# Kernel tuning notes

Hardware: AMD Instinct MI355X
Metric: run time of the kernel (lower is better)

Reference implementation:

```python
import jax, jax.numpy as jnp
import numpy as np

T, B = 384, 128
IN_DIM, HID, OUT_DIM = 512, 1024, 512


def _lstm_step(h, c, x_t, Wx, Wh, b):
    # x_t: [B, D], h/c: [B, H]; gates order: i, f, g, o
    gates = x_t @ Wx + h @ Wh + b  # [B, 4H]
    i, f, g, o = jnp.split(gates, 4, axis=-1)
    c_new = jax.nn.sigmoid(f) * c + jax.nn.sigmoid(i) * jnp.tanh(g)
    h_new = jax.nn.sigmoid(o) * jnp.tanh(c_new)
    return h_new, c_new


def setup_inputs() -> dict:
    key = jax.random.key(0)
    ks = jax.random.split(key, 9)
    s_in = 1.0 / np.sqrt(IN_DIM)
    s_h = 1.0 / np.sqrt(HID)
    s_o = 1.0 / np.sqrt(OUT_DIM)
    return {
        "x": jax.random.normal(ks[0], (T, B, IN_DIM), dtype=jnp.float32),
        "hidden_state": jnp.zeros((1, B, HID), dtype=jnp.float32),
        "cell_state": jnp.zeros((1, B, HID), dtype=jnp.float32),
        "enc_Wx": jax.random.normal(ks[1], (IN_DIM, 4 * HID), dtype=jnp.float32) * s_in,
        "enc_Wh": jax.random.normal(ks[2], (HID, 4 * HID), dtype=jnp.float32) * s_h,
        "enc_b": jnp.zeros((4 * HID,), dtype=jnp.float32),
        "dec_Wx": jax.random.normal(ks[3], (OUT_DIM, 4 * HID), dtype=jnp.float32) * s_o,
        "dec_Wh": jax.random.normal(ks[4], (HID, 4 * HID), dtype=jnp.float32) * s_h,
        "dec_b": jnp.zeros((4 * HID,), dtype=jnp.float32),
        "fc_W": jax.random.normal(ks[5], (HID, OUT_DIM), dtype=jnp.float32) * s_h,
        "fc_b": jnp.zeros((OUT_DIM,), dtype=jnp.float32),
    }


def reference(x, hidden_state, cell_state, enc_Wx, enc_Wh, enc_b,
              dec_Wx, dec_Wh, dec_b, fc_W, fc_b):
    # ---- encoder: run LSTM over T steps, keep only final hidden state ----
    h0, c0 = hidden_state[0], cell_state[0]  # [B, H]

    def enc_step(carry, x_t):
        h, c = carry
        h, c = _lstm_step(h, c, x_t, enc_Wx, enc_Wh, enc_b)
        return (h, c), None

    (h_enc, _), _ = jax.lax.scan(enc_step, (h0, c0), x)

    y0 = jnp.zeros((B, OUT_DIM), dtype=x.dtype)
    c_dec0 = jnp.zeros((B, HID), dtype=x.dtype)

    def dec_step(carry, _):
        y, h, c = carry
        h, c = _lstm_step(h, c, y, dec_Wx, dec_Wh, dec_b)
        y = jax.nn.softmax(h @ fc_W + fc_b, axis=-1)  # softmax over dim=2
        return (y, h, c), y

    _, output = jax.lax.scan(dec_step, (y0, h_enc, c_dec0), None, length=T)
    return output  # [T, B, OUT_DIM]
```

## Files before the change

### kernel.cpp

```cpp
#include <hip/hip_runtime.h>


#define TS 384

typedef __attribute__((ext_vector_type(8))) short bf16x8;
typedef __attribute__((ext_vector_type(4))) float f32x4;

#define WS_XR 4096u
#define XR_SLOT 262144u
#define WS_HP (WS_XR + 4u*XR_SLOT)
#define HP_BUF 524288u
#define WS_FPN (WS_HP + 2u*HP_BUF)
#define WS_TOTAL (WS_FPN + 2097152u)

__device__ __forceinline__ unsigned short bf16r(float v) {
  unsigned u = __float_as_uint(v);
  u += 0x7FFFu + ((u >> 16) & 1u);
  return (unsigned short)(u >> 16);
}
__device__ __forceinline__ float bf2f(unsigned short h) {
  return __uint_as_float(((unsigned)h) << 16);
}
__device__ __forceinline__ void split2(float v, short& hi, short& lo) {
  unsigned short h = bf16r(v);
  float r = v - bf2f(h);
  hi = (short)h; lo = (short)bf16r(r);
}
__device__ __forceinline__ float sigm(float v)  { return 1.0f / (1.0f + __expf(-v)); }
__device__ __forceinline__ float tanhfa(float v){ return 1.0f - 2.0f / (__expf(2.0f*v) + 1.0f); }

__device__ __forceinline__ void st_u64(short* p, unsigned long long v) {
  __hip_atomic_store((unsigned long long*)p, v, __ATOMIC_RELAXED, __HIP_MEMORY_SCOPE_AGENT);
}
__device__ __forceinline__ void st_f32(float* p, float v) {
  __hip_atomic_store(p, v, __ATOMIC_RELAXED, __HIP_MEMORY_SCOPE_AGENT);
}
__device__ __forceinline__ float ld_f32(const float* p) {
  return __hip_atomic_load(p, __ATOMIC_RELAXED, __HIP_MEMORY_SCOPE_AGENT);
}
__device__ __forceinline__ unsigned ldc(const unsigned* p) {
  return __hip_atomic_load(p, __ATOMIC_RELAXED, __HIP_MEMORY_SCOPE_AGENT);
}

__device__ __forceinline__ void arrive(unsigned* line) {
  asm volatile("s_waitcnt vmcnt(0)" ::: "memory");
  __syncthreads();
  if (threadIdx.x == 0)
    __hip_atomic_fetch_add(line, 1u, __ATOMIC_RELAXED, __HIP_MEMORY_SCOPE_AGENT);
}
__device__ __forceinline__ void wait4(const unsigned* base, unsigned target,
                                      bool fence, int* sDead) {
  if (threadIdx.x == 0) {
    unsigned spins = 0;
    for (;;) {
      unsigned c0 = ldc(base), c1 = ldc(base + 64);
      unsigned c2 = ldc(base + 128), c3 = ldc(base + 192);
      if (c0 >= target && c1 >= target && c2 >= target && c3 >= target) break;
      __builtin_amdgcn_s_sleep(1);
      if (++spins > (1u << 19)) { *sDead = 1; break; }
    }
    if (fence) __builtin_amdgcn_fence(__ATOMIC_ACQUIRE, "agent");
  }
  __syncthreads();
}
__device__ __forceinline__ void wait1(const unsigned* line, unsigned target,
                                      int* sDead) {
  if (threadIdx.x == 0) {
    unsigned spins = 0;
    while (ldc(line) < target) {
      __builtin_amdgcn_s_sleep(1);
      if (++spins > (1u << 19)) { *sDead = 1; break; }
    }
  }
  __syncthreads();
}

__device__ void load_gate_weights(const float* __restrict__ Wx, const float* __restrict__ Wh,
                                  int p, short* sBh, short* sBl) {
  for (int idx = threadIdx.x; idx < 24576; idx += 1024) {
    int j = idx & 7, l = (idx >> 3) & 63, kb = idx >> 9;
    int k = kb * 32 + ((l >> 4) << 3) + j;
    int c = l & 15;
    int gcol = (c >> 2) * 1024 + p * 4 + (c & 3);
    float wv = (k < 512) ? Wx[(size_t)k * 4096 + gcol]
                         : Wh[(size_t)(k - 512) * 4096 + gcol];
    short hi, lo; split2(wv, hi, lo);
    sBh[idx] = hi; sBl[idx] = lo;
  }
}
__device__ void load_fc_weights(const float* __restrict__ fcW, int kg, int cg,
                                short* sFh, short* sFl) {
  for (int idx = threadIdx.x; idx < 4096; idx += 1024) {
    int j = idx & 7, l = (idx >> 3) & 63, kb = idx >> 9;
    int unit = kg * 256 + kb * 32 + ((l >> 4) << 3) + j;
    int col = cg * 16 + (l & 15);
    short hi, lo; split2(fcW[(size_t)unit * 512 + col], hi, lo);
    sFh[idx] = hi; sFl[idx] = lo;
  }
}

__device__ __forceinline__ void gg(const short* AHs, const short* ALs,
    const short* BHs, const short* BLs, int mt, int l,
    int kbA0, int kbB0, int nkb, f32x4* acc)
{
  const bf16x8* AH = (const bf16x8*)AHs;
  const bf16x8* AL = (const bf16x8*)ALs;
  const bf16x8* BH = (const bf16x8*)BHs;
  const bf16x8* BL = (const bf16x8*)BLs;
  #pragma unroll 2
  for (int i = 0; i < nkb; i += 2) {
    int ka = kbA0 + i, kb = kbB0 + i;
    bf16x8 ah0 = AH[(ka * 8 + mt) * 64 + l];
    bf16x8 al0 = AL[(ka * 8 + mt) * 64 + l];
    bf16x8 bh0 = BH[kb * 64 + l];
    bf16x8 bl0 = BL[kb * 64 + l];
    bf16x8 ah1 = AH[((ka + 1) * 8 + mt) * 64 + l];
    bf16x8 al1 = AL[((ka + 1) * 8 + mt) * 64 + l];
    bf16x8 bh1 = BH[(kb + 1) * 64 + l];
    bf16x8 bl1 = BL[(kb + 1) * 64 + l];
    acc[0] = __builtin_amdgcn_mfma_f32_16x16x32_bf16(ah0, bh0, acc[0], 0, 0, 0);
    acc[1] = __builtin_amdgcn_mfma_f32_16x16x32_bf16(ah0, bl0, acc[1], 0, 0, 0);
    acc[2] = __builtin_amdgcn_mfma_f32_16x16x32_bf16(al0, bh0, acc[2], 0, 0, 0);
    acc[3] = __builtin_amdgcn_mfma_f32_16x16x32_bf16(ah1, bh1, acc[3], 0, 0, 0);
    acc[4] = __builtin_amdgcn_mfma_f32_16x16x32_bf16(ah1, bl1, acc[4], 0, 0, 0);
    acc[5] = __builtin_amdgcn_mfma_f32_16x16x32_bf16(al1, bh1, acc[5], 0, 0, 0);
  }
}
__device__ __forceinline__ void gg_finish(f32x4* acc, int kh, int mt, int l,
                                          float* LDSgate) {
  f32x4 s = (acc[0] + acc[3]) + ((acc[1] + acc[4]) + (acc[2] + acc[5]));
  const int col = l & 15, r0 = mt * 16 + ((l >> 4) << 2);
  float* plane = LDSgate + kh * 2176;
  #pragma unroll
  for (int j = 0; j < 4; ++j) plane[(r0 + j) * 17 + col] = s[j];
}

__device__ __forceinline__ void conv_x(const float* __restrict__ xsrc,
                                       short* dstH, short* dstL, int p, int t) {
  if (t < 32) {
    int g = p * 32 + t;
    int l = g & 63, mt = (g >> 6) & 7, kb = g >> 9;
    int row = mt * 16 + (l & 15), k = kb * 32 + ((l >> 4) << 3);
    const float* xs = xsrc + (size_t)row * 512 + k;
    unsigned long long h64[2] = {0, 0}, l64[2] = {0, 0};
    #pragma unroll
    for (int j = 0; j < 8; ++j) {
      short hi, lo; split2(xs[j], hi, lo);
      h64[j >> 2] |= (unsigned long long)(unsigned short)hi << ((j & 3) * 16);
      l64[j >> 2] |= (unsigned long long)(unsigned short)lo << ((j & 3) * 16);
    }
    int off = g * 8;
    st_u64(dstH + off, h64[0]); st_u64(dstH + off + 4, h64[1]);
    st_u64(dstL + off, l64[0]); st_u64(dstL + off + 4, l64[1]);
  }
}

__global__ void __launch_bounds__(1024, 1)
lstm4(const float* __restrict__ x, const float* __restrict__ h0p,
      const float* __restrict__ c0p, const float* __restrict__ eWx,
      const float* __restrict__ eWh, const float* __restrict__ eb,
      const float* __restrict__ dWx, const float* __restrict__ dWh,
      const float* __restrict__ db, const float* __restrict__ fcW,
      const float* __restrict__ fcb, float* __restrict__ out,
      char* __restrict__ ws)
{
  __shared__ __align__(16) short sBh[24576], sBl[24576];
  __shared__ __align__(16) short sFh[4096], sFl[4096];
  __shared__ float LDSgate[2 * 2176];
  __shared__ unsigned hsplit[512];
  __shared__ float ybuf[512];
  __shared__ float red[16];
  __shared__ int sDead;

  const int p = blockIdx.x, t = threadIdx.x;
  const int w = t >> 6, l = t & 63;
  const int mt = w & 7, kh = w >> 3;
  if (t == 0) sDead = 0;

  unsigned* hln = (unsigned*)ws;
  unsigned* yln = (unsigned*)(ws + 1024);
  unsigned* fln = (unsigned*)(ws + 2048);
  unsigned* my_hline = hln + (p >> 6) * 64;

  short* xrH[4]; short* xrL[4];
  #pragma unroll
  for (int s4 = 0; s4 < 4; ++s4) {
    xrH[s4] = (short*)(ws + WS_XR + s4 * XR_SLOT);
    xrL[s4] = (short*)(ws + WS_XR + s4 * XR_SLOT + 131072u);
  }
  short* hpH[2]; short* hpL[2];
  #pragma unroll
  for (int b2 = 0; b2 < 2; ++b2) {
    hpH[b2] = (short*)(ws + WS_HP + b2 * HP_BUF);
    hpL[b2] = (short*)(ws + WS_HP + b2 * HP_BUF + 262144u);
  }
  float* fp = (float*)(ws + WS_FPN);

  const int row_pw = t & 127, u_pw = (t >> 7) & 3;

  load_gate_weights(eWx, eWh, p, sBh, sBl);
  conv_x(x, xrH[0], xrL[0], p, t);
  conv_x(x + 65536, xrH[1], xrL[1], p, t);
  if (t < 64) {
    int hg = p * 64 + t;
    int ll = hg & 63, mtt = (hg >> 6) & 7, hk = hg >> 9;
    int row = mtt * 16 + (ll & 15), k = hk * 32 + ((ll >> 4) << 3);
    const float* hs = h0p + (size_t)row * 1024 + k;
    unsigned long long h64[2] = {0, 0}, l64[2] = {0, 0};
    #pragma unroll
    for (int j = 0; j < 8; ++j) {
      short hi, lo; split2(hs[j], hi, lo);
      h64[j >> 2] |= (unsigned long long)(unsigned short)hi << ((j & 3) * 16);
      l64[j >> 2] |= (unsigned long long)(unsigned short)lo << ((j & 3) * 16);
    }
    int off = hg * 8;
    st_u64(hpH[0] + off, h64[0]); st_u64(hpH[0] + off + 4, h64[1]);
    st_u64(hpL[0] + off, l64[0]); st_u64(hpL[0] + off + 4, l64[1]);
  }
  float creg = 0.f, bq0 = 0.f, bq1 = 0.f, bq2 = 0.f, bq3 = 0.f;
  if (t < 512) {
    creg = c0p[(size_t)row_pw * 1024 + p * 4 + u_pw];
    bq0 = eb[0 * 1024 + p * 4 + u_pw];
    bq1 = eb[1 * 1024 + p * 4 + u_pw];
    bq2 = eb[2 * 1024 + p * 4 + u_pw];
    bq3 = eb[3 * 1024 + p * 4 + u_pw];
  }
  arrive(my_hline);
  wait4(hln, 64u, true, &sDead);
  if (sDead) return;

  for (int st = 0; st < TS; ++st) {
    int rb = st & 1, wb = rb ^ 1, xs = st & 3;
    f32x4 z = {0.f, 0.f, 0.f, 0.f};
    f32x4 acc[6] = {z, z, z, z, z, z};
    gg(xrH[xs], xrL[xs], sBh, sBl, mt, l, kh * 8, kh * 8, 8, acc);
    wait4(hln, 64u * (st + 1), true, &sDead);
    if (sDead) return;
    gg(hpH[rb], hpL[rb], sBh, sBl, mt, l, kh * 16, 16 + kh * 16, 16, acc);
    gg_finish(acc, kh, mt, l, LDSgate);
    __syncthreads();
    if (t < 512) {
      float g0 = LDSgate[row_pw * 17 + 0  + u_pw] + LDSgate[2176 + row_pw * 17 + 0  + u_pw] + bq0;
      float g1 = LDSgate[row_pw * 17 + 4  + u_pw] + LDSgate[2176 + row_pw * 17 + 4  + u_pw] + bq1;
      float g2 = LDSgate[row_pw * 17 + 8  + u_pw] + LDSgate[2176 + row_pw * 17 + 8  + u_pw] + bq2;
      float g3 = LDSgate[row_pw * 17 + 12 + u_pw] + LDSgate[2176 + row_pw * 17 + 12 + u_pw] + bq3;
      creg = sigm(g1) * creg + sigm(g0) * tanhfa(g2);
      float h = sigm(g3) * tanhfa(creg);
      short hi, lo; split2(h, hi, lo);
      hsplit[u_pw * 128 + row_pw] = ((unsigned)(unsigned short)hi << 16) | (unsigned short)lo;
    }
    if (st + 2 < TS)
      conv_x(x + (size_t)(st + 2) * 65536, xrH[(st + 2) & 3], xrL[(st + 2) & 3], p, t);
    __syncthreads();
    if (t < 128) {
      int r = t;
      unsigned w0 = hsplit[r], w1 = hsplit[128 + r], w2 = hsplit[256 + r], w3 = hsplit[384 + r];
      unsigned long long hi64 = (unsigned long long)(w0 >> 16)
        | ((unsigned long long)(w1 >> 16) << 16)
        | ((unsigned long long)(w2 >> 16) << 32)
        | ((unsigned long long)(w3 >> 16) << 48);
      unsigned long long lo64 = (unsigned long long)(w0 & 0xFFFFu)
        | ((unsigned long long)(w1 & 0xFFFFu) << 16)
        | ((unsigned long long)(w2 & 0xFFFFu) << 32)
        | ((unsigned long long)(w3 & 0xFFFFu) << 48);
      int hk = p >> 3, mtt = r >> 4;
      int lane_ = (((p >> 1) & 3) << 4) | (r & 15);
      int off = ((hk * 8 + mtt) * 64 + lane_) * 8 + (p & 1) * 4;
      st_u64(hpH[wb] + off, hi64);
      st_u64(hpL[wb] + off, lo64);
    }
    arrive(my_hline);
  }

  load_gate_weights(dWx, dWh, p, sBh, sBl);
  if (p >= 128) load_fc_weights(fcW, (p - 128) >> 5, (p - 128) & 31, sFh, sFl);
  if (t < 32) {
    int off = (p * 32 + t) * 8;
    st_u64(xrH[0] + off, 0ull); st_u64(xrH[0] + off + 4, 0ull);
    st_u64(xrL[0] + off, 0ull); st_u64(xrL[0] + off + 4, 0ull);
  }
  creg = 0.0f;
  if (t < 512) {
    bq0 = db[0 * 1024 + p * 4 + u_pw];
    bq1 = db[1 * 1024 + p * 4 + u_pw];
    bq2 = db[2 * 1024 + p * 4 + u_pw];
    bq3 = db[3 * 1024 + p * 4 + u_pw];
  }
  float fcb_r = (t < 512) ? fcb[t] : 0.f;
  arrive(my_hline);

  const unsigned HB = (unsigned)(TS + 2);
  for (int st = 0; st < TS; ++st) {
    int rb = st & 1, wb = rb ^ 1;
    int ys = st & 1, yw = ys ^ 1;
    f32x4 z = {0.f, 0.f, 0.f, 0.f};
    f32x4 acc[6] = {z, z, z, z, z, z};
    wait4(hln, 64u * (HB + st), true, &sDead);
    if (sDead) return;
    gg(hpH[rb], hpL[rb], sBh, sBl, mt, l, kh * 16, 16 + kh * 16, 16, acc);
    wait4(yln, 32u * st, false, &sDead);
    if (sDead) return;
    gg(xrH[ys], xrL[ys], sBh, sBl, mt, l, kh * 8, kh * 8, 8, acc);
    gg_finish(acc, kh, mt, l, LDSgate);
    __syncthreads();
    if (t < 512) {
      float g0 = LDSgate[row_pw * 17 + 0  + u_pw] + LDSgate[2176 + row_pw * 17 + 0  + u_pw] + bq0;
      float g1 = LDSgate[row_pw * 17 + 4  + u_pw] + LDSgate[2176 + row_pw * 17 + 4  + u_pw] + bq1;
      float g2 = LDSgate[row_pw * 17 + 8  + u_pw] + LDSgate[2176 + row_pw * 17 + 8  + u_pw] + bq2;
      float g3 = LDSgate[row_pw * 17 + 12 + u_pw] + LDSgate[2176 + row_pw * 17 + 12 + u_pw] + bq3;
      creg = sigm(g1) * creg + sigm(g0) * tanhfa(g2);
      float h = sigm(g3) * tanhfa(creg);
      short hi, lo; split2(h, hi, lo);
      hsplit[u_pw * 128 + row_pw] = ((unsigned)(unsigned short)hi << 16) | (unsigned short)lo;
    }
    __syncthreads();
    if (t < 128) {
      int r = t;
      unsigned w0 = hsplit[r], w1 = hsplit[128 + r], w2 = hsplit[256 + r], w3 = hsplit[384 + r];
      unsigned long long hi64 = (unsigned long long)(w0 >> 16)
        | ((unsigned long long)(w1 >> 16) << 16)
        | ((unsigned long long)(w2 >> 16) << 32)
        | ((unsigned long long)(w3 >> 16) << 48);
      unsigned long long lo64 = (unsigned long long)(w0 & 0xFFFFu)
        | ((unsigned long long)(w1 & 0xFFFFu) << 16)
        | ((unsigned long long)(w2 & 0xFFFFu) << 32)
        | ((unsigned long long)(w3 & 0xFFFFu) << 48);
      int hk = p >> 3, mtt = r >> 4;
      int lane_ = (((p >> 1) & 3) << 4) | (r & 15);
      int off = ((hk * 8 + mtt) * 64 + lane_) * 8 + (p & 1) * 4;
      st_u64(hpH[wb] + off, hi64);
      st_u64(hpL[wb] + off, lo64);
    }
    arrive(my_hline);

    if (p >= 128) {
      const int f = p - 128, kg = f >> 5, cg = f & 31;
      wait1(hln + kg * 64, 64u * (HB + st + 1), &sDead);
      if (sDead) return;
      {
        const bf16x8* AH = (const bf16x8*)hpH[wb];
        const bf16x8* AL = (const bf16x8*)hpL[wb];
        const bf16x8* BH = (const bf16x8*)sFh;
        const bf16x8* BL = (const bf16x8*)sFl;
        f32x4 a0 = z, a1 = z, a2 = z;
        #pragma unroll
        for (int kb = 0; kb < 4; ++kb) {
          int hk = kg * 8 + kh * 4 + kb;
          bf16x8 ah = AH[(hk * 8 + mt) * 64 + l];
          bf16x8 al = AL[(hk * 8 + mt) * 64 + l];
          bf16x8 bh = BH[(kh * 4 + kb) * 64 + l];
          bf16x8 bl = BL[(kh * 4 + kb) * 64 + l];
          a0 = __builtin_amdgcn_mfma_f32_16x16x32_bf16(ah, bh, a0, 0, 0, 0);
          a1 = __builtin_amdgcn_mfma_f32_16x16x32_bf16(ah, bl, a1, 0, 0, 0);
          a2 = __builtin_amdgcn_mfma_f32_16x16x32_bf16(al, bh, a2, 0, 0, 0);
        }
        f32x4 s = a0 + (a1 + a2);
        int slice = kg * 2 + kh;
        int col = cg * 16 + (l & 15), r0 = mt * 16 + ((l >> 4) << 2);
        #pragma unroll
        for (int j = 0; j < 4; ++j)
          st_f32(&fp[(size_t)(slice * 128 + r0 + j) * 512 + col], s[j]);
      }
      arrive(fln + (f >> 5) * 64);
    } else {
      wait4(fln, 32u * (st + 1), false, &sDead);
      if (sDead) return;
      float v = 0.f, e = 0.f, mx;
      if (t < 512) {
        v = fcb_r;
        #pragma unroll
        for (int s8 = 0; s8 < 8; ++s8)
          v += ld_f32(&fp[(size_t)(s8 * 128 + p) * 512 + t]);
        mx = v;
        #pragma unroll
        for (int o = 32; o > 0; o >>= 1) mx = fmaxf(mx, __shfl_xor(mx, o));
        if (l == 0) red[w] = mx;
      }
      __syncthreads();
      if (t < 512) {
        mx = red[0];
        #pragma unroll
        for (int i = 1; i < 8; ++i) mx = fmaxf(mx, red[i]);
        e = __expf(v - mx);
        float ss = e;
        #pragma unroll
        for (int o = 32; o > 0; o >>= 1) ss += __shfl_xor(ss, o);
        if (l == 0) red[8 + w] = ss;
      }
      __syncthreads();
      if (t < 512) {
        float ss = (red[8] + red[9]) + (red[10] + red[11])
                 + (red[12] + red[13]) + (red[14] + red[15]);
        float y = e / ss;
        out[((size_t)st * 128 + p) * 512 + t] = y;
        ybuf[t] = y;
      }
      __syncthreads();
      if (t < 64) {
        int kb = t >> 2, seg = t & 3;
        int k = kb * 32 + seg * 8;
        int lane_ = (seg << 4) | (p & 15), mtt = p >> 4;
        int off = ((kb * 8 + mtt) * 64 + lane_) * 8;
        unsigned long long h64[2] = {0, 0}, l64[2] = {0, 0};
        #pragma unroll
        for (int j = 0; j < 8; ++j) {
          short hi, lo; split2(ybuf[k + j], hi, lo);
          h64[j >> 2] |= (unsigned long long)(unsigned short)hi << ((j & 3) * 16);
          l64[j >> 2] |= (unsigned long long)(unsigned short)lo << ((j & 3) * 16);
        }
        st_u64(xrH[yw] + off, h64[0]); st_u64(xrH[yw] + off + 4, h64[1]);
        st_u64(xrL[yw] + off, l64[0]); st_u64(xrL[yw] + off + 4, l64[1]);
      }
      arrive(yln + (p >> 5) * 64);
    }
  }
}

extern "C" void kernel_launch(void* const* d_in, const int* in_sizes, int n_in,
                              void* d_out, int out_size, void* d_ws, size_t ws_size,
                              hipStream_t stream) {
  const float* x   = (const float*)d_in[0];
  const float* h0  = (const float*)d_in[1];
  const float* c0  = (const float*)d_in[2];
  const float* eWx = (const float*)d_in[3];
  const float* eWh = (const float*)d_in[4];
  const float* eb  = (const float*)d_in[5];
  const float* dWx = (const float*)d_in[6];
  const float* dWh = (const float*)d_in[7];
  const float* db  = (const float*)d_in[8];
  const float* fcW = (const float*)d_in[9];
  const float* fcb = (const float*)d_in[10];
  float* out = (float*)d_out;

  if (ws_size < (size_t)WS_TOTAL) {
    hipMemsetAsync(d_out, 0xFF, (size_t)out_size * sizeof(float), stream);
    return;
  }
  hipMemsetAsync(d_ws, 0, 4096, stream);
  hipLaunchKernelGGL(lstm4, dim3(256), dim3(1024), 0, stream,
                     x, h0, c0, eWx, eWh, eb, dWx, dWh, db, fcW, fcb, out,
                     (char*)d_ws);
}
```

Baseline: 14.97 ms.

## Replace atomic counter barriers with per-block flags polled by a full wavefront

```diff
diff --git a/kernel.cpp b/kernel.cpp
--- a/kernel.cpp
+++ b/kernel.cpp
@@ -29,7 +29,7 @@
 __device__ __forceinline__ float sigm(float v)  { return 1.0f / (1.0f + __expf(-v)); }
 __device__ __forceinline__ float tanhfa(float v){ return 1.0f - 2.0f / (__expf(2.0f*v) + 1.0f); }
 
-__device__ __forceinline__ void st_u64(short* p, unsigned long long v) {
+__device__ __forceinline__ void st_u64(void* p, unsigned long long v) {
   __hip_atomic_store((unsigned long long*)p, v, __ATOMIC_RELAXED, __HIP_MEMORY_SCOPE_AGENT);
 }
 __device__ __forceinline__ void st_f32(float* p, float v) {
@@ -38,39 +38,42 @@
 __device__ __forceinline__ float ld_f32(const float* p) {
   return __hip_atomic_load(p, __ATOMIC_RELAXED, __HIP_MEMORY_SCOPE_AGENT);
 }
-__device__ __forceinline__ unsigned ldc(const unsigned* p) {
-  return __hip_atomic_load(p, __ATOMIC_RELAXED, __HIP_MEMORY_SCOPE_AGENT);
-}
-
-__device__ __forceinline__ void arrive(unsigned* line) {
+union FRAG { unsigned long long q[2]; bf16x8 v; };
+__device__ __forceinline__ bf16x8 ld_frag(const short* base) {
+  FRAG u;
+  u.q[0] = __hip_atomic_load((const unsigned long long*)base, __ATOMIC_RELAXED, __HIP_MEMORY_SCOPE_AGENT);
+  u.q[1] = __hip_atomic_load((const unsigned long long*)(base + 4), __ATOMIC_RELAXED, __HIP_MEMORY_SCOPE_AGENT);
+  return u.v;
+}
+
+__device__ __forceinline__ void setflag(unsigned* flag, unsigned val) {
   asm volatile("s_waitcnt vmcnt(0)" ::: "memory");
   __syncthreads();
-  if (threadIdx.x == 0)
-    __hip_atomic_fetch_add(line, 1u, __ATOMIC_RELAXED, __HIP_MEMORY_SCOPE_AGENT);
-}
-__device__ __forceinline__ void wait4(const unsigned* base, unsigned target,
-                                      bool fence, int* sDead) {
   if (threadIdx.x == 0) {
+    __hip_atomic_store(flag, val, __ATOMIC_RELAXED, __HIP_MEMORY_SCOPE_AGENT);
+    asm volatile("s_waitcnt vmcnt(0)" ::: "memory");
+  }
+}
+__device__ __forceinline__ void waitflags(const unsigned* flags, int nflags,
+                                          unsigned target, bool fence, int* sDead) {
+  if (threadIdx.x < 64) {
+    const int i = threadIdx.x;
+    const bool act = (i * 4) < nflags;
+    const unsigned long long* q = (const unsigned long long*)(flags + i * 4);
     unsigned spins = 0;
     for (;;) {
-      unsigned c0 = ldc(base), c1 = ldc(base + 64);
-      unsigned c2 = ldc(base + 128), c3 = ldc(base + 192);
-      if (c0 >= target && c1 >= target && c2 >= target && c3 >= target) break;
+      bool ok = true;
+      if (act) {
+        unsigned long long q0 = __hip_atomic_load(q, __ATOMIC_RELAXED, __HIP_MEMORY_SCOPE_AGENT);
+        unsigned long long q1 = __hip_atomic_load(q + 1, __ATOMIC_RELAXED, __HIP_MEMORY_SCOPE_AGENT);
+        ok = ((unsigned)q0 >= target) && ((unsigned)(q0 >> 32) >= target)
+          && ((unsigned)q1 >= target) && ((unsigned)(q1 >> 32) >= target);
+      }
+      if (__all(ok)) break;
       __builtin_amdgcn_s_sleep(1);
-      if (++spins > (1u << 19)) { *sDead = 1; break; }
+      if (++spins > (1u << 19)) { if (i == 0) *sDead = 1; break; }
     }
     if (fence) __builtin_amdgcn_fence(__ATOMIC_ACQUIRE, "agent");
-  }
-  __syncthreads();
-}
-__device__ __forceinline__ void wait1(const unsigned* line, unsigned target,
-                                      int* sDead) {
-  if (threadIdx.x == 0) {
-    unsigned spins = 0;
-    while (ldc(line) < target) {
-      __builtin_amdgcn_s_sleep(1);
-      if (++spins > (1u << 19)) { *sDead = 1; break; }
-    }
   }
   __syncthreads();
 }
@@ -156,7 +159,7 @@
 }
 
 __global__ void __launch_bounds__(1024, 1)
-lstm4(const float* __restrict__ x, const float* __restrict__ h0p,
+lstm6(const float* __restrict__ x, const float* __restrict__ h0p,
       const float* __restrict__ c0p, const float* __restrict__ eWx,
       const float* __restrict__ eWh, const float* __restrict__ eb,
       const float* __restrict__ dWx, const float* __restrict__ dWh,
@@ -177,10 +180,9 @@
   const int mt = w & 7, kh = w >> 3;
   if (t == 0) sDead = 0;
 
-  unsigned* hln = (unsigned*)ws;
-  unsigned* yln = (unsigned*)(ws + 1024);
-  unsigned* fln = (unsigned*)(ws + 2048);
-  unsigned* my_hline = hln + (p >> 6) * 64;
+  unsigned* hflag = (unsigned*)ws;
+  unsigned* yflag = (unsigned*)(ws + 1024);
+  unsigned* fflag = (unsigned*)(ws + 2048);
 
   short* xrH[4]; short* xrL[4];
   #pragma unroll
@@ -225,8 +227,8 @@
     bq2 = eb[2 * 1024 + p * 4 + u_pw];
     bq3 = eb[3 * 1024 + p * 4 + u_pw];
   }
-  arrive(my_hline);
-  wait4(hln, 64u, true, &sDead);
+  setflag(&hflag[p], 1u);
+  waitflags(hflag, 256, 1u, true, &sDead);
   if (sDead) return;
 
   for (int st = 0; st < TS; ++st) {
@@ -234,7 +236,7 @@
     f32x4 z = {0.f, 0.f, 0.f, 0.f};
     f32x4 acc[6] = {z, z, z, z, z, z};
     gg(xrH[xs], xrL[xs], sBh, sBl, mt, l, kh * 8, kh * 8, 8, acc);
-    wait4(hln, 64u * (st + 1), true, &sDead);
+    waitflags(hflag, 256, (unsigned)(st + 1), true, &sDead);
     if (sDead) return;
     gg(hpH[rb], hpL[rb], sBh, sBl, mt, l, kh * 16, 16 + kh * 16, 16, acc);
     gg_finish(acc, kh, mt, l, LDSgate);
@@ -269,7 +271,7 @@
       st_u64(hpH[wb] + off, hi64);
       st_u64(hpL[wb] + off, lo64);
     }
-    arrive(my_hline);
+    setflag(&hflag[p], (unsigned)(st + 2));
   }
 
   load_gate_weights(dWx, dWh, p, sBh, sBl);
@@ -287,18 +289,18 @@
     bq3 = db[3 * 1024 + p * 4 + u_pw];
   }
   float fcb_r = (t < 512) ? fcb[t] : 0.f;
-  arrive(my_hline);
-
-  const unsigned HB = (unsigned)(TS + 2);
+  setflag(&hflag[p], (unsigned)(TS + 2));
+
+  const unsigned DB = (unsigned)(TS + 2);
   for (int st = 0; st < TS; ++st) {
     int rb = st & 1, wb = rb ^ 1;
     int ys = st & 1, yw = ys ^ 1;
     f32x4 z = {0.f, 0.f, 0.f, 0.f};
     f32x4 acc[6] = {z, z, z, z, z, z};
-    wait4(hln, 64u * (HB + st), true, &sDead);
+    waitflags(hflag, 256, DB + (unsigned)st, true, &sDead);
     if (sDead) return;
     gg(hpH[rb], hpL[rb], sBh, sBl, mt, l, kh * 16, 16 + kh * 16, 16, acc);
-    wait4(yln, 32u * st, false, &sDead);
+    waitflags(yflag, 128, (unsigned)st, false, &sDead);
     if (sDead) return;
     gg(xrH[ys], xrL[ys], sBh, sBl, mt, l, kh * 8, kh * 8, 8, acc);
     gg_finish(acc, kh, mt, l, LDSgate);
@@ -331,25 +333,23 @@
       st_u64(hpH[wb] + off, hi64);
       st_u64(hpL[wb] + off, lo64);
     }
-    arrive(my_hline);
+    setflag(&hflag[p], DB + (unsigned)(st + 1));
 
     if (p >= 128) {
       const int f = p - 128, kg = f >> 5, cg = f & 31;
-      wait1(hln + kg * 64, 64u * (HB + st + 1), &sDead);
+      waitflags(hflag + kg * 64, 64, DB + (unsigned)(st + 1), false, &sDead);
       if (sDead) return;
       {
-        const bf16x8* AH = (const bf16x8*)hpH[wb];
-        const bf16x8* AL = (const bf16x8*)hpL[wb];
-        const bf16x8* BH = (const bf16x8*)sFh;
-        const bf16x8* BL = (const bf16x8*)sFl;
+        const bf16x8* FB = (const bf16x8*)sFh;
+        const bf16x8* FL = (const bf16x8*)sFl;
         f32x4 a0 = z, a1 = z, a2 = z;
         #pragma unroll
         for (int kb = 0; kb < 4; ++kb) {
-          int hk = kg * 8 + kh * 4 + kb;
-          bf16x8 ah = AH[(hk * 8 + mt) * 64 + l];
-          bf16x8 al = AL[(hk * 8 + mt) * 64 + l];
-          bf16x8 bh = BH[(kh * 4 + kb) * 64 + l];
-          bf16x8 bl = BL[(kh * 4 + kb) * 64 + l];
+          int gkb = kg * 8 + kh * 4 + kb;
+          bf16x8 ah = ld_frag(hpH[wb] + ((gkb * 8 + mt) * 64 + l) * 8);
+          bf16x8 al = ld_frag(hpL[wb] + ((gkb * 8 + mt) * 64 + l) * 8);
+          bf16x8 bh = FB[(kh * 4 + kb) * 64 + l];
+          bf16x8 bl = FL[(kh * 4 + kb) * 64 + l];
           a0 = __builtin_amdgcn_mfma_f32_16x16x32_bf16(ah, bh, a0, 0, 0, 0);
           a1 = __builtin_amdgcn_mfma_f32_16x16x32_bf16(ah, bl, a1, 0, 0, 0);
           a2 = __builtin_amdgcn_mfma_f32_16x16x32_bf16(al, bh, a2, 0, 0, 0);
@@ -361,9 +361,9 @@
         for (int j = 0; j < 4; ++j)
           st_f32(&fp[(size_t)(slice * 128 + r0 + j) * 512 + col], s[j]);
       }
-      arrive(fln + (f >> 5) * 64);
+      setflag(&fflag[f], (unsigned)(st + 1));
     } else {
-      wait4(fln, 32u * (st + 1), false, &sDead);
+      waitflags(fflag, 128, (unsigned)(st + 1), false, &sDead);
       if (sDead) return;
       float v = 0.f, e = 0.f, mx;
       if (t < 512) {
@@ -411,7 +411,7 @@
         st_u64(xrH[yw] + off, h64[0]); st_u64(xrH[yw] + off + 4, h64[1]);
         st_u64(xrL[yw] + off, l64[0]); st_u64(xrL[yw] + off + 4, l64[1]);
       }
-      arrive(yln + (p >> 5) * 64);
+      setflag(&yflag[p], (unsigned)(st + 1));
     }
   }
 }
@@ -437,7 +437,7 @@
     return;
   }
   hipMemsetAsync(d_ws, 0, 4096, stream);
-  hipLaunchKernelGGL(lstm4, dim3(256), dim3(1024), 0, stream,
+  hipLaunchKernelGGL(lstm6, dim3(256), dim3(1024), 0, stream,
                      x, h0, c0, eWx, eWh, eb, dWx, dWh, db, fcW, fcb, out,
                      (char*)d_ws);
 }
```

New measurement: 15.77 ms. +5.3%, slower.
